# Performance work log

Measured on AMD Instinct MI355X. Metric: run time of the kernel, lower is better.

The kernel has to match this reference:

```python
import jax, jax.numpy as jnp
import numpy as np

B, N, C = 1, 512, 64
CONTEXT = 3
HIDDEN = 256
N_OUT = 1
N_FEAT = C * 2 * CONTEXT  # join='cat' -> 2*C, then context shifts triple it
EPS = 1e-5


def pairing_cat(x_l, x_r, context):
    b, n, c = x_l.shape
    xl = jnp.broadcast_to(x_l[:, :, None, :], (b, n, n, c))
    xr = jnp.broadcast_to(x_r[:, None, :, :], (b, n, n, c))
    x = jnp.concatenate((xl, xr), axis=3)  # [B,N,N,2C]
    if context > 1:
        z = [x]
        for d in range(1, context // 2 + 1):
            z_u = jnp.zeros_like(x).at[:, d:, :-d, :].set(x[:, :-d, d:, :])
            z_d = jnp.zeros_like(x).at[:, :-d, d:, :].set(x[:, d:, :-d, :])
            z.append(z_u)
            z.append(z_d)
        x = jnp.concatenate(z, axis=3)  # [B,N,N,2C*context]
    return x


def setup_inputs() -> dict:
    key = jax.random.key(0)
    k = jax.random.split(key, 8)
    s1 = 1.0 / np.sqrt(N_FEAT)
    s2 = 1.0 / np.sqrt(HIDDEN)
    return {
        "x_l": jax.random.normal(k[0], (B, N, C), dtype=jnp.float32),
        "x_r": jax.random.normal(k[1], (B, N, C), dtype=jnp.float32),
        "W1": jax.random.uniform(k[2], (N_FEAT, HIDDEN), jnp.float32, -s1, s1),
        "b1": jax.random.uniform(k[3], (HIDDEN,), jnp.float32, -s1, s1),
        "gamma": jnp.ones((HIDDEN,), jnp.float32),
        "beta": jnp.zeros((HIDDEN,), jnp.float32),
        "W2": jax.random.uniform(k[4], (HIDDEN, N_OUT), jnp.float32, -s2, s2),
        "b2": jax.random.uniform(k[5], (N_OUT,), jnp.float32, -s2, s2),
    }


def reference(x_l, x_r, W1, b1, gamma, beta, W2, b2):
    x = pairing_cat(x_l, x_r, CONTEXT)  # [B,N,N,N_FEAT]
    h = jnp.einsum('bijf,fh->bijh', x, W1) + b1
    mu = jnp.mean(h, axis=-1, keepdims=True)
    var = jnp.mean(jnp.square(h - mu), axis=-1, keepdims=True)
    h = (h - mu) * jax.lax.rsqrt(var + EPS) * gamma + beta
    h = jax.nn.celu(h)  # dropout_rate=0.0 -> identity in eval/train
    y = jnp.einsum('bijh,ho->bijo', h, W2) + b2
    return y  # [B,N,N,1]
```

## Files before the change

kernel.cpp:

```cpp
#include <hip/hip_runtime.h>
#include <hip/hip_bf16.h>

#define NN  512
#define CC  64
#define HID 256
#define H4  (HID/4)
#define PSTRIDE (NN*HID)
#define PROWS 4
#define NB_BORDER 128

typedef short  bf16x8 __attribute__((ext_vector_type(8)));
typedef float  f32x4  __attribute__((ext_vector_type(4)));

__global__ __launch_bounds__(256) void proj_kernel(
    const float* __restrict__ xl, const float* __restrict__ xr,
    const float* __restrict__ W1, const float* __restrict__ b1,
    float* __restrict__ P)
{
  const int side = blockIdx.y;
  const int i0   = blockIdx.x * PROWS;
  const int h    = threadIdx.x;
  const float* __restrict__ x = side ? xr : xl;

  __shared__ float xs[PROWS][CC];
  xs[threadIdx.x >> 6][threadIdx.x & 63] = x[i0 * CC + threadIdx.x];
  __syncthreads();

  float acc0[PROWS], acc1[PROWS], acc2[PROWS];
#pragma unroll
  for (int r = 0; r < PROWS; r++) { acc0[r] = 0.f; acc1[r] = 0.f; acc2[r] = 0.f; }

  const int base = side ? CC : 0;
  const float* __restrict__ w0p = W1 + (base      ) * HID + h;
  const float* __restrict__ w1p = W1 + (base + 128) * HID + h;
  const float* __restrict__ w2p = W1 + (base + 256) * HID + h;
#pragma unroll 8
  for (int c = 0; c < CC; c++) {
    float w0 = w0p[c * HID];
    float w1 = w1p[c * HID];
    float w2 = w2p[c * HID];
#pragma unroll
    for (int r = 0; r < PROWS; r++) {
      float xv = xs[r][c];
      acc0[r] = fmaf(xv, w0, acc0[r]);
      acc1[r] = fmaf(xv, w1, acc1[r]);
      acc2[r] = fmaf(xv, w2, acc2[r]);
    }
  }

  float* __restrict__ O0 = P + (side ? 3 : 0) * PSTRIDE;
  float* __restrict__ O1 = P + (side ? 4 : 1) * PSTRIDE;
  float* __restrict__ O2 = P + (side ? 5 : 2) * PSTRIDE;
  const float bb = side ? 0.f : b1[h];
#pragma unroll
  for (int r = 0; r < PROWS; r++) {
    O0[(i0 + r) * HID + h] = acc0[r] + bb;
    O1[(i0 + r) * HID + h] = acc1[r];
    O2[(i0 + r) * HID + h] = acc2[r];
  }
}

__global__ __launch_bounds__(256) void prep_kernel(
    const float* __restrict__ P,
    float* __restrict__ Uf, float* __restrict__ Vt,
    unsigned short* __restrict__ Ubf, unsigned short* __restrict__ Vbf,
    float* __restrict__ rowstat)
{
  const int r = blockIdx.x, h = threadIdx.x;
  const float* __restrict__ PA = P;
  const float* __restrict__ PC = P + 1 * PSTRIDE;
  const float* __restrict__ PE = P + 2 * PSTRIDE;
  const float* __restrict__ PB = P + 3 * PSTRIDE;
  const float* __restrict__ PD = P + 4 * PSTRIDE;
  const float* __restrict__ PF = P + 5 * PSTRIDE;

  float u = PA[r * HID + h] + PC[(r - 1) * HID + h] + PE[(r + 1) * HID + h];
  float v = PB[r * HID + h] + PD[(r + 1) * HID + h] + PF[(r - 1) * HID + h];
  Uf[r * HID + h] = u;
  Vt[((h >> 2) * NN + r) * 4 + (h & 3)] = v;
  __hip_bfloat16 ub = __float2bfloat16(u), vb = __float2bfloat16(v);
  Ubf[r * HID + h] = *(unsigned short*)&ub;
  Vbf[r * HID + h] = *(unsigned short*)&vb;

  float u2 = u * u, v2 = v * v;
#pragma unroll
  for (int k = 32; k >= 1; k >>= 1) {
    u  += __shfl_xor(u,  k, 64);
    u2 += __shfl_xor(u2, k, 64);
    v  += __shfl_xor(v,  k, 64);
    v2 += __shfl_xor(v2, k, 64);
  }
  __shared__ float red[4][4];
  const int w = h >> 6;
  if ((h & 63) == 0) { red[w][0] = u; red[w][1] = u2; red[w][2] = v; red[w][3] = v2; }
  __syncthreads();
  if (h < 4)
    rowstat[h * NN + r] = red[0][h] + red[1][h] + red[2][h] + red[3][h];
}

__global__ __launch_bounds__(256) void cross_kernel(
    const unsigned short* __restrict__ Ubf,
    const unsigned short* __restrict__ Vbf,
    float* __restrict__ Cross)
{
  const int wave = threadIdx.x >> 6, lane = threadIdx.x & 63;
  const int t  = blockIdx.x * 4 + wave;
  const int ti = t >> 5, tj = t & 31;
  const int i0 = ti * 16, j0 = tj * 16;
  const int rc = lane & 15, kb = (lane >> 4) * 8;

  f32x4 acc = {0.f, 0.f, 0.f, 0.f};
#pragma unroll
  for (int k = 0; k < HID; k += 32) {
    bf16x8 a = *(const bf16x8*)(Ubf + (size_t)(i0 + rc) * HID + k + kb);
    bf16x8 b = *(const bf16x8*)(Vbf + (size_t)(j0 + rc) * HID + k + kb);
    acc = __builtin_amdgcn_mfma_f32_16x16x32_bf16(a, b, acc, 0, 0, 0);
  }
  const int orow = (lane >> 4) * 4, ocol = lane & 15;
#pragma unroll
  for (int r = 0; r < 4; r++)
    Cross[(size_t)(i0 + orow + r) * NN + j0 + ocol] = acc[r];
}

__device__ __forceinline__ float celu1(float x) {
  float e = __expf(x) - 1.f;
  return x > 0.f ? x : e;
}

__global__ __launch_bounds__(1024) void pair_kernel(
    const float* __restrict__ P,
    const float* __restrict__ Uf, const float* __restrict__ Vt,
    const float* __restrict__ Cross, const float* __restrict__ rowstat,
    const float* __restrict__ gamma, const float* __restrict__ beta,
    const float* __restrict__ W2, const float* __restrict__ b2,
    float* __restrict__ out)
{
  const int wave = threadIdx.x >> 6, lane = threadIdx.x & 63;
  const float b2s = b2[0];

  if (blockIdx.x >= NB_BORDER) {
    const int bx = blockIdx.x - NB_BORDER;
    const int bi = bx >> 1;
    const int i0 = 1 + (bi << 1);
    const int i1 = i0 + 1;
    const int tj = threadIdx.x & 255;
    const int hq = threadIdx.x >> 8;
    const int jj = ((bx & 1) << 8) + tj;
    const int j  = jj < 1 ? 1 : (jj > 510 ? 510 : jj);

    __shared__ __align__(16) float Gs[HID], Bs[HID], Ws[HID], U0s[HID], U1s[HID];
    __shared__ float part[3][2][256];
    if (threadIdx.x < HID) {
      Gs[threadIdx.x]  = gamma[threadIdx.x];
      Bs[threadIdx.x]  = beta[threadIdx.x];
      Ws[threadIdx.x]  = W2[threadIdx.x];
      U0s[threadIdx.x] = Uf[i0 * HID + threadIdx.x];
      U1s[threadIdx.x] = Uf[i1 * HID + threadIdx.x];
    }
    __syncthreads();

    const float inv = 1.f / HID;
    const float sV  = rowstat[2 * NN + j], sV2 = rowstat[3 * NN + j];

    const float mu0 = (rowstat[0 * NN + i0] + sV) * inv;
    const float tq0 = fmaf(2.f, Cross[i0 * NN + j], rowstat[1 * NN + i0] + sV2) * inv;
    const float rs0 = rsqrtf(tq0 - mu0 * mu0 + 1e-5f);
    const float mr0 = -mu0 * rs0;

    const float mu1 = (rowstat[0 * NN + i1] + sV) * inv;
    const float tq1 = fmaf(2.f, Cross[i1 * NN + j], rowstat[1 * NN + i1] + sV2) * inv;
    const float rs1 = rsqrtf(tq1 - mu1 * mu1 + 1e-5f);
    const float mr1 = -mu1 * rs1;

    float acc0 = 0.f, acc1 = 0.f;
    const float4* __restrict__ Vp  = (const float4*)Vt;
    const float4* __restrict__ G4  = (const float4*)Gs;
    const float4* __restrict__ B4  = (const float4*)Bs;
    const float4* __restrict__ W4  = (const float4*)Ws;
    const float4* __restrict__ U04 = (const float4*)U0s;
    const float4* __restrict__ U14 = (const float4*)U1s;

    const int hb0 = hq << 4;
#pragma unroll 4
    for (int hb = hb0; hb < hb0 + 16; hb++) {
      const float4 v4  = Vp[hb * NN + j];
      const float4 g   = G4[hb];
      const float4 be4 = B4[hb];
      const float4 w4  = W4[hb];
      const float4 u0  = U04[hb];
      const float4 u1  = U14[hb];
      {
        const float n0 = fmaf(fmaf(v4.x + u0.x, rs0, mr0), g.x, be4.x);
        acc0 = fmaf(celu1(n0), w4.x, acc0);
        const float n1 = fmaf(fmaf(v4.x + u1.x, rs1, mr1), g.x, be4.x);
        acc1 = fmaf(celu1(n1), w4.x, acc1);
      }
      {
        const float n0 = fmaf(fmaf(v4.y + u0.y, rs0, mr0), g.y, be4.y);
        acc0 = fmaf(celu1(n0), w4.y, acc0);
        const float n1 = fmaf(fmaf(v4.y + u1.y, rs1, mr1), g.y, be4.y);
        acc1 = fmaf(celu1(n1), w4.y, acc1);
      }
      {
        const float n0 = fmaf(fmaf(v4.z + u0.z, rs0, mr0), g.z, be4.z);
        acc0 = fmaf(celu1(n0), w4.z, acc0);
        const float n1 = fmaf(fmaf(v4.z + u1.z, rs1, mr1), g.z, be4.z);
        acc1 = fmaf(celu1(n1), w4.z, acc1);
      }
      {
        const float n0 = fmaf(fmaf(v4.w + u0.w, rs0, mr0), g.w, be4.w);
        acc0 = fmaf(celu1(n0), w4.w, acc0);
        const float n1 = fmaf(fmaf(v4.w + u1.w, rs1, mr1), g.w, be4.w);
        acc1 = fmaf(celu1(n1), w4.w, acc1);
      }
    }
    if (hq > 0) { part[hq - 1][0][tj] = acc0; part[hq - 1][1][tj] = acc1; }
    __syncthreads();
    if (hq == 0 && jj >= 1 && jj <= 510) {
      out[i0 * NN + jj] =
          ((acc0 + part[0][0][tj]) + (part[1][0][tj] + part[2][0][tj])) + b2s;
      out[i1 * NN + jj] =
          ((acc1 + part[0][1][tj]) + (part[1][1][tj] + part[2][1][tj])) + b2s;
    }
  } else {
    const int gw = blockIdx.x * 16 + wave;
    const float4* P4 = (const float4*)P;
    const float4* PA = P4 + 0 * (PSTRIDE / 4);
    const float4* PC = P4 + 1 * (PSTRIDE / 4);
    const float4* PE = P4 + 2 * (PSTRIDE / 4);
    const float4* PB = P4 + 3 * (PSTRIDE / 4);
    const float4* PD = P4 + 4 * (PSTRIDE / 4);
    const float4* PF = P4 + 5 * (PSTRIDE / 4);
    const float4 g  = ((const float4*)gamma)[lane];
    const float4 be = ((const float4*)beta)[lane];
    const float4 w2 = ((const float4*)W2)[lane];

    const int p = gw;
    if (p < 2044) {
      int i, j;
      if      (p < 512)  { i = 0;        j = p;        }
      else if (p < 1024) { i = 511;      j = p - 512;  }
      else if (p < 1534) { i = p - 1023; j = 0;        }
      else               { i = p - 1533; j = 511;      }

      const float4 a  = PA[i * H4 + lane];
      const float4 cu = PC[(i - 1) * H4 + lane];
      const float4 ed = PE[(i + 1) * H4 + lane];
      const float4 b  = PB[j * H4 + lane];
      const float4 du = PD[(j + 1) * H4 + lane];
      const float4 fd = PF[(j - 1) * H4 + lane];
      const float mu_m = (i >= 1 && j <= NN - 2) ? 1.f : 0.f;
      const float md_m = (i <= NN - 2 && j >= 1) ? 1.f : 0.f;

      float s0 = fmaf(md_m, ed.x + fd.x, fmaf(mu_m, cu.x + du.x, a.x + b.x));
      float s1 = fmaf(md_m, ed.y + fd.y, fmaf(mu_m, cu.y + du.y, a.y + b.y));
      float s2 = fmaf(md_m, ed.z + fd.z, fmaf(mu_m, cu.z + du.z, a.z + b.z));
      float s3 = fmaf(md_m, ed.w + fd.w, fmaf(mu_m, cu.w + du.w, a.w + b.w));

      float sum = (s0 + s1) + (s2 + s3);
      float ssq = fmaf(s0, s0, fmaf(s1, s1, fmaf(s2, s2, s3 * s3)));
#pragma unroll
      for (int off = 32; off >= 1; off >>= 1) {
        sum += __shfl_xor(sum, off, 64);
        ssq += __shfl_xor(ssq, off, 64);
      }
      const float mu  = sum * (1.f / HID);
      const float var = fmaf(ssq, 1.f / HID, -mu * mu);
      const float rs  = rsqrtf(var + 1e-5f);
      const float mrs = -mu * rs;

      auto nrm = [&](float s, float G, float Bt) {
        return fmaf(fmaf(s, rs, mrs), G, Bt);
      };
      float racc = fmaf(celu1(nrm(s0, g.x, be.x)), w2.x,
                   fmaf(celu1(nrm(s1, g.y, be.y)), w2.y,
                   fmaf(celu1(nrm(s2, g.z, be.z)), w2.z,
                        celu1(nrm(s3, g.w, be.w)) * w2.w)));
#pragma unroll
      for (int off = 32; off >= 1; off >>= 1)
        racc += __shfl_xor(racc, off, 64);
      if (lane == 0) out[i * NN + j] = racc + b2s;
    }
  }
}

extern "C" void kernel_launch(void* const* d_in, const int* in_sizes, int n_in,
                              void* d_out, int out_size, void* d_ws, size_t ws_size,
                              hipStream_t stream)
{
  const float* xl    = (const float*)d_in[0];
  const float* xr    = (const float*)d_in[1];
  const float* W1    = (const float*)d_in[2];
  const float* b1    = (const float*)d_in[3];
  const float* gamma = (const float*)d_in[4];
  const float* beta  = (const float*)d_in[5];
  const float* W2    = (const float*)d_in[6];
  const float* b2    = (const float*)d_in[7];
  float* out = (float*)d_out;

  float* P     = (float*)d_ws;
  float* Uf    = P + 6 * PSTRIDE;
  float* Vt    = Uf + NN * HID;
  float* Cross = Vt + NN * HID;
  unsigned short* Ubf = (unsigned short*)(Cross + NN * NN);
  unsigned short* Vbf = Ubf + NN * HID;
  float* rowstat = (float*)(Vbf + NN * HID);

  proj_kernel<<<dim3(NN / PROWS, 2), 256, 0, stream>>>(xl, xr, W1, b1, P);
  prep_kernel<<<NN, 256, 0, stream>>>(P, Uf, Vt, Ubf, Vbf, rowstat);
  cross_kernel<<<256, 256, 0, stream>>>(Ubf, Vbf, Cross);
  pair_kernel<<<NB_BORDER + 510, 1024, 0, stream>>>(P, Uf, Vt, Cross, rowstat,
                                                    gamma, beta, W2, b2, out);
}
```

Before: 105.6 us.

## Merge prep, cross-product and border work into one mid kernel

```diff
diff --git a/kernel.cpp b/kernel.cpp
--- a/kernel.cpp
+++ b/kernel.cpp
@@ -7,10 +7,19 @@
 #define H4  (HID/4)
 #define PSTRIDE (NN*HID)
 #define PROWS 4
-#define NB_BORDER 128
 
 typedef short  bf16x8 __attribute__((ext_vector_type(8)));
 typedef float  f32x4  __attribute__((ext_vector_type(4)));
+
+__device__ __forceinline__ short b16(float x) {
+  __hip_bfloat16 t = __float2bfloat16(x);
+  return *(short*)&t;
+}
+
+__device__ __forceinline__ float celu1(float x) {
+  float e = __expf(x) - 1.f;
+  return x > 0.f ? x : e;
+}
 
 __global__ __launch_bounds__(256) void proj_kernel(
     const float* __restrict__ xl, const float* __restrict__ xr,
@@ -60,170 +69,104 @@
   }
 }
 
-__global__ __launch_bounds__(256) void prep_kernel(
+__global__ __launch_bounds__(256) void mid_kernel(
     const float* __restrict__ P,
     float* __restrict__ Uf, float* __restrict__ Vt,
-    unsigned short* __restrict__ Ubf, unsigned short* __restrict__ Vbf,
-    float* __restrict__ rowstat)
-{
-  const int r = blockIdx.x, h = threadIdx.x;
-  const float* __restrict__ PA = P;
-  const float* __restrict__ PC = P + 1 * PSTRIDE;
-  const float* __restrict__ PE = P + 2 * PSTRIDE;
-  const float* __restrict__ PB = P + 3 * PSTRIDE;
-  const float* __restrict__ PD = P + 4 * PSTRIDE;
-  const float* __restrict__ PF = P + 5 * PSTRIDE;
-
-  float u = PA[r * HID + h] + PC[(r - 1) * HID + h] + PE[(r + 1) * HID + h];
-  float v = PB[r * HID + h] + PD[(r + 1) * HID + h] + PF[(r - 1) * HID + h];
-  Uf[r * HID + h] = u;
-  Vt[((h >> 2) * NN + r) * 4 + (h & 3)] = v;
-  __hip_bfloat16 ub = __float2bfloat16(u), vb = __float2bfloat16(v);
-  Ubf[r * HID + h] = *(unsigned short*)&ub;
-  Vbf[r * HID + h] = *(unsigned short*)&vb;
-
-  float u2 = u * u, v2 = v * v;
-#pragma unroll
-  for (int k = 32; k >= 1; k >>= 1) {
-    u  += __shfl_xor(u,  k, 64);
-    u2 += __shfl_xor(u2, k, 64);
-    v  += __shfl_xor(v,  k, 64);
-    v2 += __shfl_xor(v2, k, 64);
-  }
-  __shared__ float red[4][4];
-  const int w = h >> 6;
-  if ((h & 63) == 0) { red[w][0] = u; red[w][1] = u2; red[w][2] = v; red[w][3] = v2; }
-  __syncthreads();
-  if (h < 4)
-    rowstat[h * NN + r] = red[0][h] + red[1][h] + red[2][h] + red[3][h];
-}
-
-__global__ __launch_bounds__(256) void cross_kernel(
-    const unsigned short* __restrict__ Ubf,
-    const unsigned short* __restrict__ Vbf,
-    float* __restrict__ Cross)
-{
-  const int wave = threadIdx.x >> 6, lane = threadIdx.x & 63;
-  const int t  = blockIdx.x * 4 + wave;
-  const int ti = t >> 5, tj = t & 31;
-  const int i0 = ti * 16, j0 = tj * 16;
-  const int rc = lane & 15, kb = (lane >> 4) * 8;
-
-  f32x4 acc = {0.f, 0.f, 0.f, 0.f};
-#pragma unroll
-  for (int k = 0; k < HID; k += 32) {
-    bf16x8 a = *(const bf16x8*)(Ubf + (size_t)(i0 + rc) * HID + k + kb);
-    bf16x8 b = *(const bf16x8*)(Vbf + (size_t)(j0 + rc) * HID + k + kb);
-    acc = __builtin_amdgcn_mfma_f32_16x16x32_bf16(a, b, acc, 0, 0, 0);
-  }
-  const int orow = (lane >> 4) * 4, ocol = lane & 15;
-#pragma unroll
-  for (int r = 0; r < 4; r++)
-    Cross[(size_t)(i0 + orow + r) * NN + j0 + ocol] = acc[r];
-}
-
-__device__ __forceinline__ float celu1(float x) {
-  float e = __expf(x) - 1.f;
-  return x > 0.f ? x : e;
-}
-
-__global__ __launch_bounds__(1024) void pair_kernel(
-    const float* __restrict__ P,
-    const float* __restrict__ Uf, const float* __restrict__ Vt,
-    const float* __restrict__ Cross, const float* __restrict__ rowstat,
+    float* __restrict__ rowstat, float* __restrict__ Cross,
     const float* __restrict__ gamma, const float* __restrict__ beta,
     const float* __restrict__ W2, const float* __restrict__ b2,
     float* __restrict__ out)
 {
   const int wave = threadIdx.x >> 6, lane = threadIdx.x & 63;
-  const float b2s = b2[0];
-
-  if (blockIdx.x >= NB_BORDER) {
-    const int bx = blockIdx.x - NB_BORDER;
-    const int bi = bx >> 1;
-    const int i0 = 1 + (bi << 1);
-    const int i1 = i0 + 1;
-    const int tj = threadIdx.x & 255;
-    const int hq = threadIdx.x >> 8;
-    const int jj = ((bx & 1) << 8) + tj;
-    const int j  = jj < 1 ? 1 : (jj > 510 ? 510 : jj);
-
-    __shared__ __align__(16) float Gs[HID], Bs[HID], Ws[HID], U0s[HID], U1s[HID];
-    __shared__ float part[3][2][256];
-    if (threadIdx.x < HID) {
-      Gs[threadIdx.x]  = gamma[threadIdx.x];
-      Bs[threadIdx.x]  = beta[threadIdx.x];
-      Ws[threadIdx.x]  = W2[threadIdx.x];
-      U0s[threadIdx.x] = Uf[i0 * HID + threadIdx.x];
-      U1s[threadIdx.x] = Uf[i1 * HID + threadIdx.x];
-    }
+
+  if (blockIdx.x < 512) {
+    const int r = blockIdx.x, h = threadIdx.x;
+    const float* __restrict__ PA = P;
+    const float* __restrict__ PC = P + 1 * PSTRIDE;
+    const float* __restrict__ PE = P + 2 * PSTRIDE;
+    const float* __restrict__ PB = P + 3 * PSTRIDE;
+    const float* __restrict__ PD = P + 4 * PSTRIDE;
+    const float* __restrict__ PF = P + 5 * PSTRIDE;
+
+    float u = PA[r * HID + h] + PC[(r - 1) * HID + h] + PE[(r + 1) * HID + h];
+    float v = PB[r * HID + h] + PD[(r + 1) * HID + h] + PF[(r - 1) * HID + h];
+    Uf[r * HID + h] = u;
+    Vt[((h >> 2) * NN + r) * 4 + (h & 3)] = v;
+
+    float u2 = u * u, v2 = v * v;
+#pragma unroll
+    for (int k = 32; k >= 1; k >>= 1) {
+      u  += __shfl_xor(u,  k, 64);
+      u2 += __shfl_xor(u2, k, 64);
+      v  += __shfl_xor(v,  k, 64);
+      v2 += __shfl_xor(v2, k, 64);
+    }
+    __shared__ float red[4][4];
+    const int w = h >> 6;
+    if ((h & 63) == 0) { red[w][0] = u; red[w][1] = u2; red[w][2] = v; red[w][3] = v2; }
     __syncthreads();
-
-    const float inv = 1.f / HID;
-    const float sV  = rowstat[2 * NN + j], sV2 = rowstat[3 * NN + j];
-
-    const float mu0 = (rowstat[0 * NN + i0] + sV) * inv;
-    const float tq0 = fmaf(2.f, Cross[i0 * NN + j], rowstat[1 * NN + i0] + sV2) * inv;
-    const float rs0 = rsqrtf(tq0 - mu0 * mu0 + 1e-5f);
-    const float mr0 = -mu0 * rs0;
-
-    const float mu1 = (rowstat[0 * NN + i1] + sV) * inv;
-    const float tq1 = fmaf(2.f, Cross[i1 * NN + j], rowstat[1 * NN + i1] + sV2) * inv;
-    const float rs1 = rsqrtf(tq1 - mu1 * mu1 + 1e-5f);
-    const float mr1 = -mu1 * rs1;
-
-    float acc0 = 0.f, acc1 = 0.f;
-    const float4* __restrict__ Vp  = (const float4*)Vt;
-    const float4* __restrict__ G4  = (const float4*)Gs;
-    const float4* __restrict__ B4  = (const float4*)Bs;
-    const float4* __restrict__ W4  = (const float4*)Ws;
-    const float4* __restrict__ U04 = (const float4*)U0s;
-    const float4* __restrict__ U14 = (const float4*)U1s;
-
-    const int hb0 = hq << 4;
-#pragma unroll 4
-    for (int hb = hb0; hb < hb0 + 16; hb++) {
-      const float4 v4  = Vp[hb * NN + j];
-      const float4 g   = G4[hb];
-      const float4 be4 = B4[hb];
-      const float4 w4  = W4[hb];
-      const float4 u0  = U04[hb];
-      const float4 u1  = U14[hb];
-      {
-        const float n0 = fmaf(fmaf(v4.x + u0.x, rs0, mr0), g.x, be4.x);
-        acc0 = fmaf(celu1(n0), w4.x, acc0);
-        const float n1 = fmaf(fmaf(v4.x + u1.x, rs1, mr1), g.x, be4.x);
-        acc1 = fmaf(celu1(n1), w4.x, acc1);
-      }
-      {
-        const float n0 = fmaf(fmaf(v4.y + u0.y, rs0, mr0), g.y, be4.y);
-        acc0 = fmaf(celu1(n0), w4.y, acc0);
-        const float n1 = fmaf(fmaf(v4.y + u1.y, rs1, mr1), g.y, be4.y);
-        acc1 = fmaf(celu1(n1), w4.y, acc1);
-      }
-      {
-        const float n0 = fmaf(fmaf(v4.z + u0.z, rs0, mr0), g.z, be4.z);
-        acc0 = fmaf(celu1(n0), w4.z, acc0);
-        const float n1 = fmaf(fmaf(v4.z + u1.z, rs1, mr1), g.z, be4.z);
-        acc1 = fmaf(celu1(n1), w4.z, acc1);
-      }
-      {
-        const float n0 = fmaf(fmaf(v4.w + u0.w, rs0, mr0), g.w, be4.w);
-        acc0 = fmaf(celu1(n0), w4.w, acc0);
-        const float n1 = fmaf(fmaf(v4.w + u1.w, rs1, mr1), g.w, be4.w);
-        acc1 = fmaf(celu1(n1), w4.w, acc1);
-      }
-    }
-    if (hq > 0) { part[hq - 1][0][tj] = acc0; part[hq - 1][1][tj] = acc1; }
-    __syncthreads();
-    if (hq == 0 && jj >= 1 && jj <= 510) {
-      out[i0 * NN + jj] =
-          ((acc0 + part[0][0][tj]) + (part[1][0][tj] + part[2][0][tj])) + b2s;
-      out[i1 * NN + jj] =
-          ((acc1 + part[0][1][tj]) + (part[1][1][tj] + part[2][1][tj])) + b2s;
-    }
+    if (h < 4)
+      rowstat[h * NN + r] = red[0][h] + red[1][h] + red[2][h] + red[3][h];
+
+  } else if (blockIdx.x < 768) {
+    const int t  = (blockIdx.x - 512) * 4 + wave;
+    const int ti = t >> 5, tj = t & 31;
+    const int i0 = ti * 16, j0 = tj * 16;
+    const int rc = lane & 15, kb = (lane >> 4) * 8;
+    const int ri = i0 + rc, rj = j0 + rc;
+
+    const float4* __restrict__ PA4 = (const float4*)(P + 0 * PSTRIDE);
+    const float4* __restrict__ PC4 = (const float4*)(P + 1 * PSTRIDE);
+    const float4* __restrict__ PE4 = (const float4*)(P + 2 * PSTRIDE);
+    const float4* __restrict__ PB4 = (const float4*)(P + 3 * PSTRIDE);
+    const float4* __restrict__ PD4 = (const float4*)(P + 4 * PSTRIDE);
+    const float4* __restrict__ PF4 = (const float4*)(P + 5 * PSTRIDE);
+
+    f32x4 acc = {0.f, 0.f, 0.f, 0.f};
+#pragma unroll
+    for (int k = 0; k < HID; k += 32) {
+      const int hu = (ri * HID + k + kb) >> 2;
+      const int hc = ((ri - 1) * HID + k + kb) >> 2;
+      const int he = ((ri + 1) * HID + k + kb) >> 2;
+      const float4 a0 = PA4[hu],     a1 = PA4[hu + 1];
+      const float4 c0 = PC4[hc],     c1 = PC4[hc + 1];
+      const float4 e0 = PE4[he],     e1 = PE4[he + 1];
+
+      const int hv = (rj * HID + k + kb) >> 2;
+      const int hd = ((rj + 1) * HID + k + kb) >> 2;
+      const int hf = ((rj - 1) * HID + k + kb) >> 2;
+      const float4 b0 = PB4[hv],     b1v = PB4[hv + 1];
+      const float4 d0 = PD4[hd],     d1 = PD4[hd + 1];
+      const float4 f0 = PF4[hf],     f1 = PF4[hf + 1];
+
+      bf16x8 ua, vb;
+      ua[0] = b16(a0.x + c0.x + e0.x);
+      ua[1] = b16(a0.y + c0.y + e0.y);
+      ua[2] = b16(a0.z + c0.z + e0.z);
+      ua[3] = b16(a0.w + c0.w + e0.w);
+      ua[4] = b16(a1.x + c1.x + e1.x);
+      ua[5] = b16(a1.y + c1.y + e1.y);
+      ua[6] = b16(a1.z + c1.z + e1.z);
+      ua[7] = b16(a1.w + c1.w + e1.w);
+      vb[0] = b16(b0.x + d0.x + f0.x);
+      vb[1] = b16(b0.y + d0.y + f0.y);
+      vb[2] = b16(b0.z + d0.z + f0.z);
+      vb[3] = b16(b0.w + d0.w + f0.w);
+      vb[4] = b16(b1v.x + d1.x + f1.x);
+      vb[5] = b16(b1v.y + d1.y + f1.y);
+      vb[6] = b16(b1v.z + d1.z + f1.z);
+      vb[7] = b16(b1v.w + d1.w + f1.w);
+
+      acc = __builtin_amdgcn_mfma_f32_16x16x32_bf16(ua, vb, acc, 0, 0, 0);
+    }
+    const int orow = (lane >> 4) * 4, ocol = lane & 15;
+#pragma unroll
+    for (int r = 0; r < 4; r++)
+      Cross[(size_t)(i0 + orow + r) * NN + j0 + ocol] = acc[r];
+
   } else {
-    const int gw = blockIdx.x * 16 + wave;
+    const int gw = (blockIdx.x - 768) * 4 + wave;
+    const float b2s = b2[0];
     const float4* P4 = (const float4*)P;
     const float4* PA = P4 + 0 * (PSTRIDE / 4);
     const float4* PC = P4 + 1 * (PSTRIDE / 4);
@@ -235,8 +178,10 @@
     const float4 be = ((const float4*)beta)[lane];
     const float4 w2 = ((const float4*)W2)[lane];
 
-    const int p = gw;
-    if (p < 2044) {
+#pragma unroll
+    for (int tt = 0; tt < 2; tt++) {
+      const int p = gw * 2 + tt;
+      if (p >= 2044) break;
       int i, j;
       if      (p < 512)  { i = 0;        j = p;        }
       else if (p < 1024) { i = 511;      j = p - 512;  }
@@ -281,6 +226,100 @@
         racc += __shfl_xor(racc, off, 64);
       if (lane == 0) out[i * NN + j] = racc + b2s;
     }
+  }
+}
+
+__global__ __launch_bounds__(1024) void pair_kernel(
+    const float* __restrict__ Uf, const float* __restrict__ Vt,
+    const float* __restrict__ Cross, const float* __restrict__ rowstat,
+    const float* __restrict__ gamma, const float* __restrict__ beta,
+    const float* __restrict__ W2, const float* __restrict__ b2,
+    float* __restrict__ out)
+{
+  const float b2s = b2[0];
+
+  const int bx = blockIdx.x;
+  const int bi = bx >> 1;
+  const int i0 = 1 + (bi << 1);
+  const int i1 = i0 + 1;
+  const int tj = threadIdx.x & 255;
+  const int hq = threadIdx.x >> 8;
+  const int jj = ((bx & 1) << 8) + tj;
+  const int j  = jj < 1 ? 1 : (jj > 510 ? 510 : jj);
+
+  __shared__ __align__(16) float Gs[HID], Bs[HID], Ws[HID], U0s[HID], U1s[HID];
+  __shared__ float part[3][2][256];
+  if (threadIdx.x < HID) {
+    Gs[threadIdx.x]  = gamma[threadIdx.x];
+    Bs[threadIdx.x]  = beta[threadIdx.x];
+    Ws[threadIdx.x]  = W2[threadIdx.x];
+    U0s[threadIdx.x] = Uf[i0 * HID + threadIdx.x];
+    U1s[threadIdx.x] = Uf[i1 * HID + threadIdx.x];
+  }
+  __syncthreads();
+
+  const float inv = 1.f / HID;
+  const float sV  = rowstat[2 * NN + j], sV2 = rowstat[3 * NN + j];
+
+  const float mu0 = (rowstat[0 * NN + i0] + sV) * inv;
+  const float tq0 = fmaf(2.f, Cross[i0 * NN + j], rowstat[1 * NN + i0] + sV2) * inv;
+  const float rs0 = rsqrtf(tq0 - mu0 * mu0 + 1e-5f);
+  const float mr0 = -mu0 * rs0;
+
+  const float mu1 = (rowstat[0 * NN + i1] + sV) * inv;
+  const float tq1 = fmaf(2.f, Cross[i1 * NN + j], rowstat[1 * NN + i1] + sV2) * inv;
+  const float rs1 = rsqrtf(tq1 - mu1 * mu1 + 1e-5f);
+  const float mr1 = -mu1 * rs1;
+
+  float acc0 = 0.f, acc1 = 0.f;
+  const float4* __restrict__ Vp  = (const float4*)Vt;
+  const float4* __restrict__ G4  = (const float4*)Gs;
+  const float4* __restrict__ B4  = (const float4*)Bs;
+  const float4* __restrict__ W4  = (const float4*)Ws;
+  const float4* __restrict__ U04 = (const float4*)U0s;
+  const float4* __restrict__ U14 = (const float4*)U1s;
+
+  const int hb0 = hq << 4;
+#pragma unroll 4
+  for (int hb = hb0; hb < hb0 + 16; hb++) {
+    const float4 v4  = Vp[hb * NN + j];
+    const float4 g   = G4[hb];
+    const float4 be4 = B4[hb];
+    const float4 w4  = W4[hb];
+    const float4 u0  = U04[hb];
+    const float4 u1  = U14[hb];
+    {
+      const float n0 = fmaf(fmaf(v4.x + u0.x, rs0, mr0), g.x, be4.x);
+      acc0 = fmaf(celu1(n0), w4.x, acc0);
+      const float n1 = fmaf(fmaf(v4.x + u1.x, rs1, mr1), g.x, be4.x);
+      acc1 = fmaf(celu1(n1), w4.x, acc1);
+    }
+    {
+      const float n0 = fmaf(fmaf(v4.y + u0.y, rs0, mr0), g.y, be4.y);
+      acc0 = fmaf(celu1(n0), w4.y, acc0);
+      const float n1 = fmaf(fmaf(v4.y + u1.y, rs1, mr1), g.y, be4.y);
+      acc1 = fmaf(celu1(n1), w4.y, acc1);
+    }
+    {
+      const float n0 = fmaf(fmaf(v4.z + u0.z, rs0, mr0), g.z, be4.z);
+      acc0 = fmaf(celu1(n0), w4.z, acc0);
+      const float n1 = fmaf(fmaf(v4.z + u1.z, rs1, mr1), g.z, be4.z);
+      acc1 = fmaf(celu1(n1), w4.z, acc1);
+    }
+    {
+      const float n0 = fmaf(fmaf(v4.w + u0.w, rs0, mr0), g.w, be4.w);
+      acc0 = fmaf(celu1(n0), w4.w, acc0);
+      const float n1 = fmaf(fmaf(v4.w + u1.w, rs1, mr1), g.w, be4.w);
+      acc1 = fmaf(celu1(n1), w4.w, acc1);
+    }
+  }
+  if (hq > 0) { part[hq - 1][0][tj] = acc0; part[hq - 1][1][tj] = acc1; }
+  __syncthreads();
+  if (hq == 0 && jj >= 1 && jj <= 510) {
+    out[i0 * NN + jj] =
+        ((acc0 + part[0][0][tj]) + (part[1][0][tj] + part[2][0][tj])) + b2s;
+    out[i1 * NN + jj] =
+        ((acc1 + part[0][1][tj]) + (part[1][1][tj] + part[2][1][tj])) + b2s;
   }
 }
 
@@ -298,17 +337,15 @@
   const float* b2    = (const float*)d_in[7];
   float* out = (float*)d_out;
 
-  float* P     = (float*)d_ws;
-  float* Uf    = P + 6 * PSTRIDE;
-  float* Vt    = Uf + NN * HID;
-  float* Cross = Vt + NN * HID;
-  unsigned short* Ubf = (unsigned short*)(Cross + NN * NN);
-  unsigned short* Vbf = Ubf + NN * HID;
-  float* rowstat = (float*)(Vbf + NN * HID);
+  float* P       = (float*)d_ws;
+  float* Uf      = P + 6 * PSTRIDE;
+  float* Vt      = Uf + NN * HID;
+  float* Cross   = Vt + NN * HID;
+  float* rowstat = Cross + NN * NN;
 
   proj_kernel<<<dim3(NN / PROWS, 2), 256, 0, stream>>>(xl, xr, W1, b1, P);
-  prep_kernel<<<NN, 256, 0, stream>>>(P, Uf, Vt, Ubf, Vbf, rowstat);
-  cross_kernel<<<256, 256, 0, stream>>>(Ubf, Vbf, Cross);
-  pair_kernel<<<NB_BORDER + 510, 1024, 0, stream>>>(P, Uf, Vt, Cross, rowstat,
-                                                    gamma, beta, W2, b2, out);
-}
+  mid_kernel<<<1024, 256, 0, stream>>>(P, Uf, Vt, rowstat, Cross,
+                                       gamma, beta, W2, b2, out);
+  pair_kernel<<<510, 1024, 0, stream>>>(Uf, Vt, Cross, rowstat,
+                                        gamma, beta, W2, b2, out);
+}
```

After: 113.0 us. 7.0% more time.

## Fuse cross-term dot product into pair kernel, drop bf16 MFMA cross kernel

Applied to the files above, without the earlier changes.

```diff
diff --git a/kernel.cpp b/kernel.cpp
--- a/kernel.cpp
+++ b/kernel.cpp
@@ -9,8 +9,12 @@
 #define PROWS 4
 #define NB_BORDER 128
 
-typedef short  bf16x8 __attribute__((ext_vector_type(8)));
 typedef float  f32x4  __attribute__((ext_vector_type(4)));
+
+__device__ __forceinline__ float celu1(float x) {
+  float e = __expf(x) - 1.f;
+  return x > 0.f ? x : e;
+}
 
 __global__ __launch_bounds__(256) void proj_kernel(
     const float* __restrict__ xl, const float* __restrict__ xr,
@@ -63,7 +67,6 @@
 __global__ __launch_bounds__(256) void prep_kernel(
     const float* __restrict__ P,
     float* __restrict__ Uf, float* __restrict__ Vt,
-    unsigned short* __restrict__ Ubf, unsigned short* __restrict__ Vbf,
     float* __restrict__ rowstat)
 {
   const int r = blockIdx.x, h = threadIdx.x;
@@ -78,9 +81,6 @@
   float v = PB[r * HID + h] + PD[(r + 1) * HID + h] + PF[(r - 1) * HID + h];
   Uf[r * HID + h] = u;
   Vt[((h >> 2) * NN + r) * 4 + (h & 3)] = v;
-  __hip_bfloat16 ub = __float2bfloat16(u), vb = __float2bfloat16(v);
-  Ubf[r * HID + h] = *(unsigned short*)&ub;
-  Vbf[r * HID + h] = *(unsigned short*)&vb;
 
   float u2 = u * u, v2 = v * v;
 #pragma unroll
@@ -98,39 +98,10 @@
     rowstat[h * NN + r] = red[0][h] + red[1][h] + red[2][h] + red[3][h];
 }
 
-__global__ __launch_bounds__(256) void cross_kernel(
-    const unsigned short* __restrict__ Ubf,
-    const unsigned short* __restrict__ Vbf,
-    float* __restrict__ Cross)
-{
-  const int wave = threadIdx.x >> 6, lane = threadIdx.x & 63;
-  const int t  = blockIdx.x * 4 + wave;
-  const int ti = t >> 5, tj = t & 31;
-  const int i0 = ti * 16, j0 = tj * 16;
-  const int rc = lane & 15, kb = (lane >> 4) * 8;
-
-  f32x4 acc = {0.f, 0.f, 0.f, 0.f};
-#pragma unroll
-  for (int k = 0; k < HID; k += 32) {
-    bf16x8 a = *(const bf16x8*)(Ubf + (size_t)(i0 + rc) * HID + k + kb);
-    bf16x8 b = *(const bf16x8*)(Vbf + (size_t)(j0 + rc) * HID + k + kb);
-    acc = __builtin_amdgcn_mfma_f32_16x16x32_bf16(a, b, acc, 0, 0, 0);
-  }
-  const int orow = (lane >> 4) * 4, ocol = lane & 15;
-#pragma unroll
-  for (int r = 0; r < 4; r++)
-    Cross[(size_t)(i0 + orow + r) * NN + j0 + ocol] = acc[r];
-}
-
-__device__ __forceinline__ float celu1(float x) {
-  float e = __expf(x) - 1.f;
-  return x > 0.f ? x : e;
-}
-
-__global__ __launch_bounds__(1024) void pair_kernel(
+__global__ __launch_bounds__(1024, 8) void pair_kernel(
     const float* __restrict__ P,
     const float* __restrict__ Uf, const float* __restrict__ Vt,
-    const float* __restrict__ Cross, const float* __restrict__ rowstat,
+    const float* __restrict__ rowstat,
     const float* __restrict__ gamma, const float* __restrict__ beta,
     const float* __restrict__ W2, const float* __restrict__ b2,
     float* __restrict__ out)
@@ -149,7 +120,7 @@
     const int j  = jj < 1 ? 1 : (jj > 510 ? 510 : jj);
 
     __shared__ __align__(16) float Gs[HID], Bs[HID], Ws[HID], U0s[HID], U1s[HID];
-    __shared__ float part[3][2][256];
+    __shared__ float red[4][2][256];
     if (threadIdx.x < HID) {
       Gs[threadIdx.x]  = gamma[threadIdx.x];
       Bs[threadIdx.x]  = beta[threadIdx.x];
@@ -159,28 +130,43 @@
     }
     __syncthreads();
 
-    const float inv = 1.f / HID;
-    const float sV  = rowstat[2 * NN + j], sV2 = rowstat[3 * NN + j];
-
-    const float mu0 = (rowstat[0 * NN + i0] + sV) * inv;
-    const float tq0 = fmaf(2.f, Cross[i0 * NN + j], rowstat[1 * NN + i0] + sV2) * inv;
-    const float rs0 = rsqrtf(tq0 - mu0 * mu0 + 1e-5f);
-    const float mr0 = -mu0 * rs0;
-
-    const float mu1 = (rowstat[0 * NN + i1] + sV) * inv;
-    const float tq1 = fmaf(2.f, Cross[i1 * NN + j], rowstat[1 * NN + i1] + sV2) * inv;
-    const float rs1 = rsqrtf(tq1 - mu1 * mu1 + 1e-5f);
-    const float mr1 = -mu1 * rs1;
-
-    float acc0 = 0.f, acc1 = 0.f;
     const float4* __restrict__ Vp  = (const float4*)Vt;
     const float4* __restrict__ G4  = (const float4*)Gs;
     const float4* __restrict__ B4  = (const float4*)Bs;
     const float4* __restrict__ W4  = (const float4*)Ws;
     const float4* __restrict__ U04 = (const float4*)U0s;
     const float4* __restrict__ U14 = (const float4*)U1s;
-
     const int hb0 = hq << 4;
+
+    float d0 = 0.f, d1 = 0.f;
+#pragma unroll 4
+    for (int hb = hb0; hb < hb0 + 16; hb++) {
+      const float4 v4 = Vp[hb * NN + j];
+      const float4 u0 = U04[hb];
+      const float4 u1 = U14[hb];
+      d0 = fmaf(v4.x, u0.x, fmaf(v4.y, u0.y, fmaf(v4.z, u0.z, fmaf(v4.w, u0.w, d0))));
+      d1 = fmaf(v4.x, u1.x, fmaf(v4.y, u1.y, fmaf(v4.z, u1.z, fmaf(v4.w, u1.w, d1))));
+    }
+    red[hq][0][tj] = d0;
+    red[hq][1][tj] = d1;
+    __syncthreads();
+    const float dot0 = (red[0][0][tj] + red[1][0][tj]) + (red[2][0][tj] + red[3][0][tj]);
+    const float dot1 = (red[0][1][tj] + red[1][1][tj]) + (red[2][1][tj] + red[3][1][tj]);
+
+    const float inv = 1.f / HID;
+    const float sV  = rowstat[2 * NN + j], sV2 = rowstat[3 * NN + j];
+
+    const float mu0 = (rowstat[0 * NN + i0] + sV) * inv;
+    const float tq0 = fmaf(2.f, dot0, rowstat[1 * NN + i0] + sV2) * inv;
+    const float rs0 = rsqrtf(tq0 - mu0 * mu0 + 1e-5f);
+    const float mr0 = -mu0 * rs0;
+
+    const float mu1 = (rowstat[0 * NN + i1] + sV) * inv;
+    const float tq1 = fmaf(2.f, dot1, rowstat[1 * NN + i1] + sV2) * inv;
+    const float rs1 = rsqrtf(tq1 - mu1 * mu1 + 1e-5f);
+    const float mr1 = -mu1 * rs1;
+
+    float acc0 = 0.f, acc1 = 0.f;
 #pragma unroll 4
     for (int hb = hb0; hb < hb0 + 16; hb++) {
       const float4 v4  = Vp[hb * NN + j];
@@ -214,13 +200,14 @@
         acc1 = fmaf(celu1(n1), w4.w, acc1);
       }
     }
-    if (hq > 0) { part[hq - 1][0][tj] = acc0; part[hq - 1][1][tj] = acc1; }
+    __syncthreads();
+    if (hq > 0) { red[hq][0][tj] = acc0; red[hq][1][tj] = acc1; }
     __syncthreads();
     if (hq == 0 && jj >= 1 && jj <= 510) {
       out[i0 * NN + jj] =
-          ((acc0 + part[0][0][tj]) + (part[1][0][tj] + part[2][0][tj])) + b2s;
+          ((acc0 + red[1][0][tj]) + (red[2][0][tj] + red[3][0][tj])) + b2s;
       out[i1 * NN + jj] =
-          ((acc1 + part[0][1][tj]) + (part[1][1][tj] + part[2][1][tj])) + b2s;
+          ((acc1 + red[1][1][tj]) + (red[2][1][tj] + red[3][1][tj])) + b2s;
     }
   } else {
     const int gw = blockIdx.x * 16 + wave;
@@ -298,17 +285,13 @@
   const float* b2    = (const float*)d_in[7];
   float* out = (float*)d_out;
 
-  float* P     = (float*)d_ws;
-  float* Uf    = P + 6 * PSTRIDE;
-  float* Vt    = Uf + NN * HID;
-  float* Cross = Vt + NN * HID;
-  unsigned short* Ubf = (unsigned short*)(Cross + NN * NN);
-  unsigned short* Vbf = Ubf + NN * HID;
-  float* rowstat = (float*)(Vbf + NN * HID);
+  float* P       = (float*)d_ws;
+  float* Uf      = P + 6 * PSTRIDE;
+  float* Vt      = Uf + NN * HID;
+  float* rowstat = Vt + NN * HID;
 
   proj_kernel<<<dim3(NN / PROWS, 2), 256, 0, stream>>>(xl, xr, W1, b1, P);
-  prep_kernel<<<NN, 256, 0, stream>>>(P, Uf, Vt, Ubf, Vbf, rowstat);
-  cross_kernel<<<256, 256, 0, stream>>>(Ubf, Vbf, Cross);
-  pair_kernel<<<NB_BORDER + 510, 1024, 0, stream>>>(P, Uf, Vt, Cross, rowstat,
+  prep_kernel<<<NN, 256, 0, stream>>>(P, Uf, Vt, rowstat);
+  pair_kernel<<<NB_BORDER + 510, 1024, 0, stream>>>(P, Uf, Vt, rowstat,
                                                     gamma, beta, W2, b2, out);
 }
```

After: 104.4 us. No clear change (-1.1%).
